# Kernel tuning notes

Measured on AMD Instinct MI355X. Metric: run time of the kernel, lower is better.

## Reference

```python
import jax, jax.numpy as jnp
import numpy as np

NUM_HEADS = 8
DIM = 256  # == out_dim; module implicitly requires dim == out_dim


def setup_inputs() -> dict:
    key = jax.random.key(0)
    k0, k1, k2, k3, k4, k5 = jax.random.split(key, 6)
    B, N, T, dim = 4, 128, 128, DIM
    s = dim ** -0.5
    return {
        "v": jax.random.normal(k0, (B, N, T, dim), dtype=jnp.float32),
        "Wq": jax.random.normal(k1, (dim, dim), dtype=jnp.float32) * s,
        "Wk": jax.random.normal(k2, (dim, dim), dtype=jnp.float32) * s,
        "Wv": jax.random.normal(k3, (dim, dim), dtype=jnp.float32) * s,
        "Wp": jax.random.normal(k4, (dim, dim), dtype=jnp.float32) * s,
        "bp": jax.random.normal(k5, (dim,), dtype=jnp.float32) * 0.01,
    }


def reference(v, Wq, Wk, Wv, Wp, bp):
    B, N, T, dim = v.shape
    H = NUM_HEADS
    hd = dim // H
    scale = hd ** -0.5
    # projections (qkv_bias=False)
    q = (v @ Wq).reshape(B * N, T, H, hd)
    k = (v @ Wk).reshape(B * N, T, H, hd)
    vv = (v @ Wv).reshape(B * N, T, H, hd)
    # NOTE: heads axis is NOT moved before the matmul in the original torch
    # code, so attention is over the HEADS axis: per (b*n, t) an HxH matrix.
    attn = jnp.einsum('mthd,mtgd->mthg', q, k) * scale  # [B*N, T, H, H]
    attn = jax.nn.softmax(attn, axis=-1)
    x = jnp.einsum('mthg,mtgd->mthd', attn, vv).reshape(B, N, T, dim)
    # output projection (with bias); dropout probs are 0 / eval mode
    return x @ Wp + bp
```

## Files before the change

### kernel.cpp

```cpp
#include <hip/hip_runtime.h>
#include <hip/hip_bf16.h>
#include <math.h>


#define DIMX      256
#define NH        8
#define HD        32
#define TM        48
#define NTHREADS  512
#define QSTRIDE   776
#define KT        8
#define NT_QKV    48

typedef _Float16 f16x8 __attribute__((ext_vector_type(8)));
typedef _Float16 f16x4 __attribute__((ext_vector_type(4)));
typedef _Float16 f16x2 __attribute__((ext_vector_type(2)));
typedef float    f32x4 __attribute__((ext_vector_type(4)));

static __device__ __forceinline__ f16x2 pkrtz(float a, float b) {
    return (f16x2)__builtin_amdgcn_cvt_pkrtz(a, b);
}

__global__ void pack_weights(const float* __restrict__ Wq,
                             const float* __restrict__ Wk,
                             const float* __restrict__ Wv,
                             const float* __restrict__ Wp,
                             _Float16* __restrict__ pk)
{
    const int QKV_FRAGS = NT_QKV * KT * 64;
    int u = blockIdx.x * blockDim.x + threadIdx.x;
    const float* W;
    int nt, kt, lane;
    if (u < QKV_FRAGS) {
        nt = u / (KT * 64); kt = (u / 64) % KT; lane = u % 64;
        if (nt < 16)      { W = Wq; }
        else if (nt < 32) { W = Wk; nt -= 16; }
        else              { W = Wv; nt -= 32; }
    } else {
        int u2 = u - QKV_FRAGS;
        nt = u2 / (KT * 64); kt = (u2 / 64) % KT; lane = u2 % 64;
        W = Wp;
    }
    const int n  = nt * 16 + (lane & 15);
    const int k0 = kt * 32 + (lane >> 4) * 8;
    f16x8 frag;
#pragma unroll
    for (int j = 0; j < 8; ++j)
        frag[j] = (_Float16)W[(size_t)(k0 + j) * DIMX + n];
    *(f16x8*)(pk + (size_t)u * 8) = frag;
}

__global__ __launch_bounds__(NTHREADS, 2)
void fused_attn_mfma(const float* __restrict__ v,
                     const _Float16* __restrict__ Wqkv_pk,
                     const _Float16* __restrict__ Wp_pk,
                     const float* __restrict__ bp,
                     float* __restrict__ out,
                     int ntok)
{
    __shared__ __align__(16) _Float16 S[TM * QSTRIDE];

    const int tid   = threadIdx.x;
    const int lane  = tid & 63;
    const int wv_id = tid >> 6;
    const int l15   = lane & 15;
    const int quad  = lane >> 4;
    const int token0 = blockIdx.x * TM;
    int valid = ntok - token0; if (valid > TM) valid = TM;

    const int tiles0[3] = { 16 + 3 * wv_id, 17 + 3 * wv_id, 18 + 3 * wv_id };
    const int tiles1[3] = { 2 * wv_id, 2 * wv_id + 1, 40 + wv_id };

    const f16x8* wb  = (const f16x8*)Wqkv_pk + lane;
    const f16x8* wb2 = (const f16x8*)Wp_pk + lane;

    {
        const float4* src = (const float4*)(v + (size_t)token0 * DIMX);
        float4 t4[6];
#pragma unroll
        for (int i = 0; i < 6; ++i) {
            int u = tid + NTHREADS * i;
            int m = u >> 6;
            t4[i] = (m < valid) ? src[u] : (float4){0.f, 0.f, 0.f, 0.f};
        }
#pragma unroll
        for (int i = 0; i < 6; ++i) {
            int u = tid + NTHREADS * i;
            int m = u >> 6;
            int c = (u & 63) * 4;
            f16x2 lo = pkrtz(t4[i].x, t4[i].y), hi = pkrtz(t4[i].z, t4[i].w);
            f16x4 b4 = { lo.x, lo.y, hi.x, hi.y };
            *(f16x4*)&S[m * QSTRIDE + c] = b4;
        }
    }
    f16x8 wA[3], wB[3];
#pragma unroll
    for (int j = 0; j < 3; ++j) wA[j] = wb[(size_t)(tiles0[j] * KT + 0) * 64];
#pragma unroll
    for (int j = 0; j < 3; ++j) wB[j] = wb[(size_t)(tiles0[j] * KT + 1) * 64];
    __syncthreads();

    f32x4 acc0[3][3];
#pragma unroll
    for (int j = 0; j < 3; ++j)
#pragma unroll
        for (int tt = 0; tt < 3; ++tt)
            acc0[j][tt] = (f32x4){0.f, 0.f, 0.f, 0.f};

#pragma unroll
    for (int kt = 0; kt < KT; ++kt) {
        f16x8 wC[3];
        if (kt < KT - 2) {
#pragma unroll
            for (int j = 0; j < 3; ++j)
                wC[j] = wb[(size_t)(tiles0[j] * KT + kt + 2) * 64];
        } else {
#pragma unroll
            for (int j = 0; j < 3; ++j) wC[j] = wB[j];
        }
        f16x8 vf[3];
#pragma unroll
        for (int tt = 0; tt < 3; ++tt)
            vf[tt] = *(const f16x8*)&S[(tt * 16 + l15) * QSTRIDE + kt * 32 + quad * 8];
#pragma unroll
        for (int j = 0; j < 3; ++j)
#pragma unroll
            for (int tt = 0; tt < 3; ++tt)
                acc0[j][tt] = __builtin_amdgcn_mfma_f32_16x16x32_f16(wA[j], vf[tt], acc0[j][tt], 0, 0, 0);
#pragma unroll
        for (int j = 0; j < 3; ++j) { wA[j] = wB[j]; wB[j] = wC[j]; }
    }

    f16x8 pA[3], pB[3];
#pragma unroll
    for (int j = 0; j < 3; ++j) pA[j] = wb[(size_t)(tiles1[j] * KT + 0) * 64];
#pragma unroll
    for (int j = 0; j < 3; ++j) pB[j] = wb[(size_t)(tiles1[j] * KT + 1) * 64];

#pragma unroll
    for (int j = 0; j < 3; ++j)
#pragma unroll
        for (int tt = 0; tt < 3; ++tt) {
            f16x2 a = pkrtz(acc0[j][tt][0], acc0[j][tt][1]);
            f16x2 b = pkrtz(acc0[j][tt][2], acc0[j][tt][3]);
            f16x4 p4 = { a.x, a.y, b.x, b.y };
            *(f16x4*)&S[(tt * 16 + l15) * QSTRIDE + tiles0[j] * 16 + quad * 4] = p4;
        }

    f32x4 acc1[3][3];
#pragma unroll
    for (int j = 0; j < 3; ++j)
#pragma unroll
        for (int tt = 0; tt < 3; ++tt)
            acc1[j][tt] = (f32x4){0.f, 0.f, 0.f, 0.f};

#pragma unroll
    for (int kt = 0; kt < KT; ++kt) {
        f16x8 pC[3];
        if (kt < KT - 2) {
#pragma unroll
            for (int j = 0; j < 3; ++j)
                pC[j] = wb[(size_t)(tiles1[j] * KT + kt + 2) * 64];
        } else {
#pragma unroll
            for (int j = 0; j < 3; ++j) pC[j] = pB[j];
        }
        f16x8 vf[3];
#pragma unroll
        for (int tt = 0; tt < 3; ++tt)
            vf[tt] = *(const f16x8*)&S[(tt * 16 + l15) * QSTRIDE + kt * 32 + quad * 8];
#pragma unroll
        for (int j = 0; j < 3; ++j)
#pragma unroll
            for (int tt = 0; tt < 3; ++tt)
                acc1[j][tt] = __builtin_amdgcn_mfma_f32_16x16x32_f16(pA[j], vf[tt], acc1[j][tt], 0, 0, 0);
#pragma unroll
        for (int j = 0; j < 3; ++j) { pA[j] = pB[j]; pB[j] = pC[j]; }
    }
    __syncthreads();

#pragma unroll
    for (int j = 0; j < 3; ++j)
#pragma unroll
        for (int tt = 0; tt < 3; ++tt) {
            f16x2 a = pkrtz(acc1[j][tt][0], acc1[j][tt][1]);
            f16x2 b = pkrtz(acc1[j][tt][2], acc1[j][tt][3]);
            f16x4 p4 = { a.x, a.y, b.x, b.y };
            *(f16x4*)&S[(tt * 16 + l15) * QSTRIDE + tiles1[j] * 16 + quad * 4] = p4;
        }

    const int nt0 = 2 * wv_id;
    f16x8 wA2[2], wB2[2];
#pragma unroll
    for (int j = 0; j < 2; ++j) wA2[j] = wb2[(size_t)((nt0 + j) * KT + 0) * 64];
#pragma unroll
    for (int j = 0; j < 2; ++j) wB2[j] = wb2[(size_t)((nt0 + j) * KT + 1) * 64];
    __syncthreads();

    const int ta  = tid >> 3;
    const int h   = tid & 7;
    const bool act = (ta < TM);
    f16x8 xa0, xa1, xa2, xa3;
    if (act) {
        const float scale = 0.17677669529663687f;
        const _Float16* qrow  = &S[ta * QSTRIDE + h * HD];
        const _Float16* kbase = &S[ta * QSTRIDE + 256];
        const _Float16* vbase = &S[ta * QSTRIDE + 512];

        f16x8 q0 = *(const f16x8*)(qrow);
        f16x8 q1 = *(const f16x8*)(qrow + 8);
        f16x8 q2 = *(const f16x8*)(qrow + 16);
        f16x8 q3 = *(const f16x8*)(qrow + 24);

        float logits[NH];
#pragma unroll
        for (int g = 0; g < NH; ++g) {
            const _Float16* kg = kbase + g * HD;
            f16x8 p = q0 * *(const f16x8*)(kg);
            p += q1 * *(const f16x8*)(kg + 8);
            p += q2 * *(const f16x8*)(kg + 16);
            p += q3 * *(const f16x8*)(kg + 24);
            f16x4 r4 = __builtin_shufflevector(p, p, 0, 1, 2, 3)
                     + __builtin_shufflevector(p, p, 4, 5, 6, 7);
            f16x2 r2 = __builtin_shufflevector(r4, r4, 0, 1)
                     + __builtin_shufflevector(r4, r4, 2, 3);
            logits[g] = ((float)r2.x + (float)r2.y) * scale;
        }
        float mx = logits[0];
#pragma unroll
        for (int g = 1; g < NH; ++g) mx = fmaxf(mx, logits[g]);
        float se = 0.f;
#pragma unroll
        for (int g = 0; g < NH; ++g) { logits[g] = __expf(logits[g] - mx); se += logits[g]; }
        float inv = 1.f / se;

        xa0 = (f16x8)(_Float16)0.f; xa1 = (f16x8)(_Float16)0.f;
        xa2 = (f16x8)(_Float16)0.f; xa3 = (f16x8)(_Float16)0.f;
#pragma unroll
        for (int g = 0; g < NH; ++g) {
            _Float16 ph = (_Float16)(logits[g] * inv);
            f16x8 pw = { ph, ph, ph, ph, ph, ph, ph, ph };
            const _Float16* vg = vbase + g * HD;
            xa0 += pw * *(const f16x8*)(vg);
            xa1 += pw * *(const f16x8*)(vg + 8);
            xa2 += pw * *(const f16x8*)(vg + 16);
            xa3 += pw * *(const f16x8*)(vg + 24);
        }
    }
    __syncthreads();
    if (act) {
        _Float16* xrow = &S[ta * QSTRIDE + h * HD];
        *(f16x8*)(xrow)      = xa0;
        *(f16x8*)(xrow + 8)  = xa1;
        *(f16x8*)(xrow + 16) = xa2;
        *(f16x8*)(xrow + 24) = xa3;
    }
    __syncthreads();

    {
        f32x4 acc2[2][3];
#pragma unroll
        for (int j = 0; j < 2; ++j)
#pragma unroll
            for (int tt = 0; tt < 3; ++tt)
                acc2[j][tt] = (f32x4){0.f, 0.f, 0.f, 0.f};

#pragma unroll
        for (int kt = 0; kt < KT; ++kt) {
            f16x8 wC2[2];
            if (kt < KT - 2) {
#pragma unroll
                for (int j = 0; j < 2; ++j)
                    wC2[j] = wb2[(size_t)((nt0 + j) * KT + kt + 2) * 64];
            } else {
#pragma unroll
                for (int j = 0; j < 2; ++j) wC2[j] = wB2[j];
            }
            f16x8 xf[3];
#pragma unroll
            for (int tt = 0; tt < 3; ++tt)
                xf[tt] = *(const f16x8*)&S[(tt * 16 + l15) * QSTRIDE + kt * 32 + quad * 8];
#pragma unroll
            for (int j = 0; j < 2; ++j)
#pragma unroll
                for (int tt = 0; tt < 3; ++tt)
                    acc2[j][tt] = __builtin_amdgcn_mfma_f32_16x16x32_f16(wA2[j], xf[tt], acc2[j][tt], 0, 0, 0);
#pragma unroll
            for (int j = 0; j < 2; ++j) { wA2[j] = wB2[j]; wB2[j] = wC2[j]; }
        }

#pragma unroll
        for (int j = 0; j < 2; ++j) {
            f32x4 b = *(const f32x4*)&bp[(nt0 + j) * 16 + quad * 4];
#pragma unroll
            for (int tt = 0; tt < 3; ++tt) {
                int row = token0 + tt * 16 + l15;
                if (row < ntok) {
                    f32x4 o = acc2[j][tt] + b;
                    *(f32x4*)&out[(size_t)row * DIMX + (nt0 + j) * 16 + quad * 4] = o;
                }
            }
        }
    }
}

extern "C" void kernel_launch(void* const* d_in, const int* in_sizes, int n_in,
                              void* d_out, int out_size, void* d_ws, size_t ws_size,
                              hipStream_t stream) {
    const float* v  = (const float*)d_in[0];
    const float* Wq = (const float*)d_in[1];
    const float* Wk = (const float*)d_in[2];
    const float* Wv = (const float*)d_in[3];
    const float* Wp = (const float*)d_in[4];
    const float* bp = (const float*)d_in[5];
    float* out = (float*)d_out;

    _Float16* pk = (_Float16*)d_ws;
    const _Float16* Wqkv_pk = pk;
    const _Float16* Wp_pk   = pk + (size_t)24576 * 8;

    pack_weights<<<256, 128, 0, stream>>>(Wq, Wk, Wv, Wp, pk);

    const int ntokens = in_sizes[0] / DIMX;
    const int nblk = (ntokens + TM - 1) / TM;
    fused_attn_mfma<<<nblk, NTHREADS, 0, stream>>>(v, Wqkv_pk, Wp_pk, bp, out, ntokens);
}
```

Baseline: 154.9 us.

## Keep Q in registers aligned with head tiles, shrink shared buffer

Each wave's N-tile assignment is rearranged so it computes exactly the Q tiles for its head (wave w owns head w). Q then stays in MFMA accumulator registers, and attention is done with lane shuffles across the quad dimension instead of a per-(token, head) thread mapping. This drops the shared-memory row stride from 776 to 520 halves by storing only K and V, with X reusing the space freed by the input and K, and raises the occupancy hint to 6 blocks. The aim is less LDS traffic and footprint and more resident blocks, at the cost of extra shuffles, more register pressure, and fp32 dot products in the attention step.

After: 305.1 us. 1.97x slower.

```diff
diff --git a/kernel.cpp b/kernel.cpp
--- a/kernel.cpp
+++ b/kernel.cpp
@@ -8,7 +8,7 @@
 #define HD        32
 #define TM        48
 #define NTHREADS  512
-#define QSTRIDE   776
+#define QS        520
 #define KT        8
 #define NT_QKV    48
 
@@ -19,6 +19,10 @@
 
 static __device__ __forceinline__ f16x2 pkrtz(float a, float b) {
     return (f16x2)__builtin_amdgcn_cvt_pkrtz(a, b);
+}
+static __device__ __forceinline__ f16x4 pk4(const f32x4& a) {
+    f16x2 lo = pkrtz(a[0], a[1]), hi = pkrtz(a[2], a[3]);
+    return (f16x4){ lo.x, lo.y, hi.x, hi.y };
 }
 
 __global__ void pack_weights(const float* __restrict__ Wq,
@@ -50,7 +54,7 @@
     *(f16x8*)(pk + (size_t)u * 8) = frag;
 }
 
-__global__ __launch_bounds__(NTHREADS, 2)
+__global__ __launch_bounds__(NTHREADS, 6)
 void fused_attn_mfma(const float* __restrict__ v,
                      const _Float16* __restrict__ Wqkv_pk,
                      const _Float16* __restrict__ Wp_pk,
@@ -58,7 +62,7 @@
                      float* __restrict__ out,
                      int ntok)
 {
-    __shared__ __align__(16) _Float16 S[TM * QSTRIDE];
+    __shared__ __align__(16) _Float16 S[TM * QS];
 
     const int tid   = threadIdx.x;
     const int lane  = tid & 63;
@@ -68,8 +72,8 @@
     const int token0 = blockIdx.x * TM;
     int valid = ntok - token0; if (valid > TM) valid = TM;
 
-    const int tiles0[3] = { 16 + 3 * wv_id, 17 + 3 * wv_id, 18 + 3 * wv_id };
-    const int tiles1[3] = { 2 * wv_id, 2 * wv_id + 1, 40 + wv_id };
+    const int tiles0[3] = { 16 + 2 * wv_id, 17 + 2 * wv_id, 32 + 2 * wv_id };
+    const int tiles1[3] = { 2 * wv_id, 2 * wv_id + 1, 33 + 2 * wv_id };
 
     const f16x8* wb  = (const f16x8*)Wqkv_pk + lane;
     const f16x8* wb2 = (const f16x8*)Wp_pk + lane;
@@ -90,7 +94,7 @@
             int c = (u & 63) * 4;
             f16x2 lo = pkrtz(t4[i].x, t4[i].y), hi = pkrtz(t4[i].z, t4[i].w);
             f16x4 b4 = { lo.x, lo.y, hi.x, hi.y };
-            *(f16x4*)&S[m * QSTRIDE + c] = b4;
+            *(f16x4*)&S[m * QS + 256 + c] = b4;
         }
     }
     f16x8 wA[3], wB[3];
@@ -121,7 +125,7 @@
         f16x8 vf[3];
 #pragma unroll
         for (int tt = 0; tt < 3; ++tt)
-            vf[tt] = *(const f16x8*)&S[(tt * 16 + l15) * QSTRIDE + kt * 32 + quad * 8];
+            vf[tt] = *(const f16x8*)&S[(tt * 16 + l15) * QS + 256 + kt * 32 + quad * 8];
 #pragma unroll
         for (int j = 0; j < 3; ++j)
 #pragma unroll
@@ -137,15 +141,14 @@
 #pragma unroll
     for (int j = 0; j < 3; ++j) pB[j] = wb[(size_t)(tiles1[j] * KT + 1) * 64];
 
-#pragma unroll
-    for (int j = 0; j < 3; ++j)
-#pragma unroll
-        for (int tt = 0; tt < 3; ++tt) {
-            f16x2 a = pkrtz(acc0[j][tt][0], acc0[j][tt][1]);
-            f16x2 b = pkrtz(acc0[j][tt][2], acc0[j][tt][3]);
-            f16x4 p4 = { a.x, a.y, b.x, b.y };
-            *(f16x4*)&S[(tt * 16 + l15) * QSTRIDE + tiles0[j] * 16 + quad * 4] = p4;
-        }
+    f16x4 pend0[3];
+#pragma unroll
+    for (int j = 0; j < 2; ++j)
+#pragma unroll
+        for (int tt = 0; tt < 3; ++tt)
+            *(f16x4*)&S[(tt * 16 + l15) * QS + (tiles0[j] - 16) * 16 + quad * 4] = pk4(acc0[j][tt]);
+#pragma unroll
+    for (int tt = 0; tt < 3; ++tt) pend0[tt] = pk4(acc0[2][tt]);
 
     f32x4 acc1[3][3];
 #pragma unroll
@@ -168,7 +171,7 @@
         f16x8 vf[3];
 #pragma unroll
         for (int tt = 0; tt < 3; ++tt)
-            vf[tt] = *(const f16x8*)&S[(tt * 16 + l15) * QSTRIDE + kt * 32 + quad * 8];
+            vf[tt] = *(const f16x8*)&S[(tt * 16 + l15) * QS + 256 + kt * 32 + quad * 8];
 #pragma unroll
         for (int j = 0; j < 3; ++j)
 #pragma unroll
@@ -177,17 +180,14 @@
 #pragma unroll
         for (int j = 0; j < 3; ++j) { pA[j] = pB[j]; pB[j] = pC[j]; }
     }
-    __syncthreads();
-
-#pragma unroll
-    for (int j = 0; j < 3; ++j)
-#pragma unroll
-        for (int tt = 0; tt < 3; ++tt) {
-            f16x2 a = pkrtz(acc1[j][tt][0], acc1[j][tt][1]);
-            f16x2 b = pkrtz(acc1[j][tt][2], acc1[j][tt][3]);
-            f16x4 p4 = { a.x, a.y, b.x, b.y };
-            *(f16x4*)&S[(tt * 16 + l15) * QSTRIDE + tiles1[j] * 16 + quad * 4] = p4;
-        }
+
+    f16x4 qf0[3], qf1[3], pend1[3];
+#pragma unroll
+    for (int tt = 0; tt < 3; ++tt) {
+        qf0[tt]   = pk4(acc1[0][tt]);
+        qf1[tt]   = pk4(acc1[1][tt]);
+        pend1[tt] = pk4(acc1[2][tt]);
+    }
 
     const int nt0 = 2 * wv_id;
     f16x8 wA2[2], wB2[2];
@@ -195,65 +195,72 @@
     for (int j = 0; j < 2; ++j) wA2[j] = wb2[(size_t)((nt0 + j) * KT + 0) * 64];
 #pragma unroll
     for (int j = 0; j < 2; ++j) wB2[j] = wb2[(size_t)((nt0 + j) * KT + 1) * 64];
-    __syncthreads();
-
-    const int ta  = tid >> 3;
-    const int h   = tid & 7;
-    const bool act = (ta < TM);
-    f16x8 xa0, xa1, xa2, xa3;
-    if (act) {
+
+    __syncthreads();
+
+#pragma unroll
+    for (int tt = 0; tt < 3; ++tt) {
+        *(f16x4*)&S[(tt * 16 + l15) * QS + 256 + 32 * wv_id + quad * 4]      = pend0[tt];
+        *(f16x4*)&S[(tt * 16 + l15) * QS + 256 + 32 * wv_id + 16 + quad * 4] = pend1[tt];
+    }
+    __syncthreads();
+
+    f16x4 xq0[3], xq1[3];
+    {
         const float scale = 0.17677669529663687f;
-        const _Float16* qrow  = &S[ta * QSTRIDE + h * HD];
-        const _Float16* kbase = &S[ta * QSTRIDE + 256];
-        const _Float16* vbase = &S[ta * QSTRIDE + 512];
-
-        f16x8 q0 = *(const f16x8*)(qrow);
-        f16x8 q1 = *(const f16x8*)(qrow + 8);
-        f16x8 q2 = *(const f16x8*)(qrow + 16);
-        f16x8 q3 = *(const f16x8*)(qrow + 24);
-
-        float logits[NH];
-#pragma unroll
-        for (int g = 0; g < NH; ++g) {
-            const _Float16* kg = kbase + g * HD;
-            f16x8 p = q0 * *(const f16x8*)(kg);
-            p += q1 * *(const f16x8*)(kg + 8);
-            p += q2 * *(const f16x8*)(kg + 16);
-            p += q3 * *(const f16x8*)(kg + 24);
-            f16x4 r4 = __builtin_shufflevector(p, p, 0, 1, 2, 3)
-                     + __builtin_shufflevector(p, p, 4, 5, 6, 7);
-            f16x2 r2 = __builtin_shufflevector(r4, r4, 0, 1)
-                     + __builtin_shufflevector(r4, r4, 2, 3);
-            logits[g] = ((float)r2.x + (float)r2.y) * scale;
-        }
-        float mx = logits[0];
-#pragma unroll
-        for (int g = 1; g < NH; ++g) mx = fmaxf(mx, logits[g]);
-        float se = 0.f;
-#pragma unroll
-        for (int g = 0; g < NH; ++g) { logits[g] = __expf(logits[g] - mx); se += logits[g]; }
-        float inv = 1.f / se;
-
-        xa0 = (f16x8)(_Float16)0.f; xa1 = (f16x8)(_Float16)0.f;
-        xa2 = (f16x8)(_Float16)0.f; xa3 = (f16x8)(_Float16)0.f;
-#pragma unroll
-        for (int g = 0; g < NH; ++g) {
-            _Float16 ph = (_Float16)(logits[g] * inv);
-            f16x8 pw = { ph, ph, ph, ph, ph, ph, ph, ph };
-            const _Float16* vg = vbase + g * HD;
-            xa0 += pw * *(const f16x8*)(vg);
-            xa1 += pw * *(const f16x8*)(vg + 8);
-            xa2 += pw * *(const f16x8*)(vg + 16);
-            xa3 += pw * *(const f16x8*)(vg + 24);
-        }
-    }
-    __syncthreads();
-    if (act) {
-        _Float16* xrow = &S[ta * QSTRIDE + h * HD];
-        *(f16x8*)(xrow)      = xa0;
-        *(f16x8*)(xrow + 8)  = xa1;
-        *(f16x8*)(xrow + 16) = xa2;
-        *(f16x8*)(xrow + 24) = xa3;
+#pragma unroll
+        for (int tt = 0; tt < 3; ++tt) {
+            const int t = tt * 16 + l15;
+            const _Float16* krow = &S[t * QS];
+            const _Float16* vrow = &S[t * QS + 256];
+
+            float lg[NH];
+#pragma unroll
+            for (int g = 0; g < NH; ++g) {
+                f16x4 ka = *(const f16x4*)&krow[g * HD + quad * 4];
+                f16x4 kb = *(const f16x4*)&krow[g * HD + 16 + quad * 4];
+                float p = 0.f;
+#pragma unroll
+                for (int r = 0; r < 4; ++r)
+                    p += (float)qf0[tt][r] * (float)ka[r]
+                       + (float)qf1[tt][r] * (float)kb[r];
+                p += __shfl_xor(p, 16, 64);
+                p += __shfl_xor(p, 32, 64);
+                lg[g] = p * scale;
+            }
+            float mx = lg[0];
+#pragma unroll
+            for (int g = 1; g < NH; ++g) mx = fmaxf(mx, lg[g]);
+            float se = 0.f;
+#pragma unroll
+            for (int g = 0; g < NH; ++g) { lg[g] = __expf(lg[g] - mx); se += lg[g]; }
+            float inv = 1.f / se;
+
+            float xr0[4] = {0.f, 0.f, 0.f, 0.f};
+            float xr1[4] = {0.f, 0.f, 0.f, 0.f};
+#pragma unroll
+            for (int g = 0; g < NH; ++g) {
+                f16x4 va = *(const f16x4*)&vrow[g * HD + quad * 4];
+                f16x4 vb = *(const f16x4*)&vrow[g * HD + 16 + quad * 4];
+                float w8 = lg[g] * inv;
+#pragma unroll
+                for (int r = 0; r < 4; ++r) {
+                    xr0[r] += w8 * (float)va[r];
+                    xr1[r] += w8 * (float)vb[r];
+                }
+            }
+            f16x2 a0 = pkrtz(xr0[0], xr0[1]), b0 = pkrtz(xr0[2], xr0[3]);
+            f16x2 a1 = pkrtz(xr1[0], xr1[1]), b1 = pkrtz(xr1[2], xr1[3]);
+            xq0[tt] = (f16x4){ a0.x, a0.y, b0.x, b0.y };
+            xq1[tt] = (f16x4){ a1.x, a1.y, b1.x, b1.y };
+        }
+    }
+    __syncthreads();
+#pragma unroll
+    for (int tt = 0; tt < 3; ++tt) {
+        const int t = tt * 16 + l15;
+        *(f16x4*)&S[t * QS + 32 * wv_id + quad * 4]      = xq0[tt];
+        *(f16x4*)&S[t * QS + 32 * wv_id + 16 + quad * 4] = xq1[tt];
     }
     __syncthreads();
 
@@ -279,7 +286,7 @@
             f16x8 xf[3];
 #pragma unroll
             for (int tt = 0; tt < 3; ++tt)
-                xf[tt] = *(const f16x8*)&S[(tt * 16 + l15) * QSTRIDE + kt * 32 + quad * 8];
+                xf[tt] = *(const f16x8*)&S[(tt * 16 + l15) * QS + kt * 32 + quad * 8];
 #pragma unroll
             for (int j = 0; j < 2; ++j)
 #pragma unroll
```
